# Performance work log

Hardware: AMD Instinct MI355X
Metric: run time of the kernel (lower is better)

The kernel has to match this reference:

```python
import jax, jax.numpy as jnp
import numpy as np

DIM = 256      # d_model (MCMoE default dim=256)
E = 4          # experts: [CoAFusion, SNNFusion, DAMISLFusion, DropX2Fusion]
K = 2          # max_experts (top-k in cosine gate)
ATT = 128      # gated-attention hidden dim in DAMISL MIL pooling
N1, N2, B = 16384, 4096, 1


def setup_inputs() -> dict:
    key = jax.random.key(0)
    ks = jax.random.split(key, 16)
    s = 1.0 / np.sqrt(DIM)
    f32 = jnp.float32
    lin = lambda k, shape, scale: jax.random.normal(k, shape, f32) * scale
    return {
        'x1': jax.random.normal(ks[0], (B, N1, DIM), f32),
        'x2': jax.random.normal(ks[1], (B, N2, DIM), f32),
        # MM_CosineGate params: per-expert prototype rows + activation thresholds
        'sim_matrix': lin(ks[2], (E, DIM), 1.0),
        'gates': jnp.zeros((E,), f32),
        # SNNFusion: RMSNorm scales + two SNN blocks (Linear+ELU)
        'g1': jnp.ones((DIM,), f32),
        'g2': jnp.ones((DIM,), f32),
        'snn_w1': lin(ks[3], (DIM, DIM), s), 'snn_b1': jnp.zeros((DIM,), f32),
        'snn_w2': lin(ks[4], (DIM, DIM), s), 'snn_b2': jnp.zeros((DIM,), f32),
        # CoAFusion: single-head cross attention x1 -> x2
        'wq': lin(ks[5], (DIM, DIM), s), 'wk': lin(ks[6], (DIM, DIM), s),
        'wv': lin(ks[7], (DIM, DIM), s), 'wo': lin(ks[8], (DIM, DIM), s),
        # DAMISLFusion: gated-attention MIL pooling over x2 + fuse linear
        'va': lin(ks[9], (DIM, ATT), s), 'ua': lin(ks[10], (DIM, ATT), s),
        'wa': lin(ks[11], (ATT, 1), 1.0 / np.sqrt(ATT)),
        'wf': lin(ks[12], (DIM, DIM), s),
    }


def _rms(x, g):
    return x * jax.lax.rsqrt(jnp.mean(x * x, axis=-1, keepdims=True) + 1e-6) * g


def _forward(x1, x2, sim_matrix, gates, g1, g2, snn_w1, snn_b1, snn_w2, snn_b2,
             wq, wk, wv, wo, va, ua, wa, wf):
    # ---- MM_CosineGate: cosine similarity of pooled multimodal feature vs prototypes
    f = 0.5 * (x1.mean(axis=1) + x2.mean(axis=1))                       # [B, D]
    fn = f * jax.lax.rsqrt(jnp.sum(f * f, -1, keepdims=True) + 1e-8)
    sn = sim_matrix * jax.lax.rsqrt(jnp.sum(sim_matrix * sim_matrix, -1, keepdims=True) + 1e-8)
    scores = fn @ sn.T                                                  # [B, E]
    topv = jax.lax.top_k(scores, K)[0]                                  # [B, K]
    keep = (scores >= topv[:, -1:]) & (scores > gates[None, :])         # top-k AND above gate
    logits = jnp.where(keep, scores, 0.0)                               # [B, E], 0 for inactive

    # ---- Expert 0: CoAFusion (cross attention, residual)
    attn = jax.nn.softmax(
        jnp.einsum('bnd,bmd->bnm', x1 @ wq, x2 @ wk) / np.sqrt(DIM), axis=-1)  # [B, N1, N2]
    e0 = x1 + jnp.einsum('bnm,bmd->bnd', attn, x2 @ wv) @ wo

    # ---- Expert 1: SNNFusion (per-token SNN on x1 + pooled SNN on x2)
    e1 = jax.nn.elu(_rms(x1, g1) @ snn_w1 + snn_b1) \
         + jax.nn.elu(_rms(x2, g2) @ snn_w2 + snn_b2).mean(axis=1, keepdims=True)

    # ---- Expert 2: DAMISLFusion (gated-attention MIL pool of x2, broadcast fuse)
    h = jnp.tanh(x2 @ va) * jax.nn.sigmoid(x2 @ ua)                     # [B, N2, ATT]
    a = jax.nn.softmax((h @ wa)[..., 0], axis=1)                        # [B, N2]
    pooled = jnp.einsum('bm,bmd->bd', a, x2)                            # [B, D]
    e2 = x1 + (pooled @ wf)[:, None, :]

    # ---- Expert 3: DropX2Fusion (identity on x1)
    e3 = x1

    # ---- Weighted combine over selected experts (weight 0 => expert contributes 0),
    # then divide by number of selected experts (matches `outputs /= num_selected`).
    w = logits
    out = (w[:, 0, None, None] * e0 + w[:, 1, None, None] * e1
           + w[:, 2, None, None] * e2 + w[:, 3, None, None] * e3)
    num_sel = jnp.maximum(jnp.sum(logits > 0, axis=-1), 1).astype(out.dtype)  # [B]
    return out / num_sel[:, None, None]


def reference(x1, x2, sim_matrix, gates, g1, g2, snn_w1, snn_b1, snn_w2, snn_b2,
              wq, wk, wv, wo, va, ua, wa, wf):
    return _forward(x1, x2, sim_matrix, gates, g1, g2, snn_w1, snn_b1,
                    snn_w2, snn_b2, wq, wk, wv, wo, va, ua, wa, wf)
```

## Files before the change

### kernel.cpp

```cpp
#include <hip/hip_runtime.h>
#include <math.h>

#define N1 16384
#define N2 4096
#define DIM 256
#define ATT 128

typedef unsigned int uint32;
typedef __attribute__((ext_vector_type(4))) short s4v;
typedef __attribute__((ext_vector_type(8))) short s8v;
typedef __attribute__((ext_vector_type(16))) float f16v;
typedef __attribute__((ext_vector_type(2))) uint32 u2v;
typedef __attribute__((ext_vector_type(4))) uint32 u4v;

union S8U { s8v v; s4v h[2]; };

#define AS1C const __attribute__((address_space(1)))
#define AS3 __attribute__((address_space(3)))

#define WS_KPK 0
#define WS_VPK 524288
#define WS_WQT 1048576
#define WS_WOT 1081344
#define WS_W1T 1114112
#define WS_WKT 1146880
#define WS_WVT 1179648
#define WS_W2T 1212416
#define WS_VAT 1245184
#define WS_UAT 1261568
#define WS_ACC 1277952
#define WS_COLSUM1 (WS_ACC)
#define WS_COLSUM2 (WS_ACC+256)
#define WS_S2SUM  (WS_ACC+512)
#define WS_POOLED (WS_ACC+768)
#define WS_SUME   (WS_ACC+1024)
#define WS_GATE   (WS_ACC+1040)

#define L_K    0
#define L_V    65536
#define L_P    131072
#define L_LP   147456
#define L_LINV 149504
#define L_RRS  149760
#define L_RR   150016
#define L_CVL  150272
#define L_X1PK  0
#define L_QPAD  65536
#define L_OBUF  0
#define L_X1PK2 65536
#define SMEM_BYTES 151296

__device__ __forceinline__ uint32 f2bf1(float f) {
    uint32 u = __float_as_uint(f);
    return (u + 0x7fffu + ((u >> 16) & 1u)) >> 16;
}
__device__ __forceinline__ uint32 f2bf2(float lo, float hi) {
    return f2bf1(lo) | (f2bf1(hi) << 16);
}
#define MFMA32(a, b, c) __builtin_amdgcn_mfma_f32_32x32x16_bf16((a), (b), (c), 0, 0, 0)

__global__ __launch_bounds__(256) void k_pre(const float* __restrict__ x1,
    const float* __restrict__ x2,
    const float* __restrict__ wq, const float* __restrict__ wo,
    const float* __restrict__ snn_w1, const float* __restrict__ wk,
    const float* __restrict__ wv, const float* __restrict__ snn_w2,
    const float* __restrict__ va, const float* __restrict__ ua,
    const float* __restrict__ g1, const float* __restrict__ g2,
    float* __restrict__ ws)
{
    const int b = blockIdx.x;
    const int t = threadIdx.x;
    if (b < 224) {
        int mat, chunk, ncols;
        if (b < 192) { mat = b >> 5; chunk = b & 31; ncols = 256; }
        else { mat = 6 + ((b - 192) >> 4); chunk = (b - 192) & 15; ncols = 128; }
        const float* W;
        int dstoff;
        switch (mat) {
            case 0: W = wq;     dstoff = WS_WQT; break;
            case 1: W = wo;     dstoff = WS_WOT; break;
            case 2: W = snn_w1; dstoff = WS_W1T; break;
            case 3: W = wk;     dstoff = WS_WKT; break;
            case 4: W = wv;     dstoff = WS_WVT; break;
            case 5: W = snn_w2; dstoff = WS_W2T; break;
            case 6: W = va;     dstoff = WS_VAT; break;
            default: W = ua;    dstoff = WS_UAT; break;
        }
        unsigned short* dst = (unsigned short*)(ws + dstoff);
        const int e0 = chunk * 2048 + t * 8;
        const int k = (ncols == 256) ? (e0 >> 8) : (e0 >> 7);
        const int n0 = (ncols == 256) ? (e0 & 255) : (e0 & 127);
        const float4 v0 = *(const float4*)(W + k * ncols + n0);
        const float4 v1 = *(const float4*)(W + k * ncols + n0 + 4);
        const float sc = (mat == 2) ? g1[k] : ((mat == 5) ? g2[k] : 1.0f);
        float vals[8] = {v0.x, v0.y, v0.z, v0.w, v1.x, v1.y, v1.z, v1.w};
        const unsigned int sbase = (unsigned int)(k >> 4) * 512u
            + 32u * ((k >> 3) & 1) * 8u + (k & 7);
        #pragma unroll
        for (int jj = 0; jj < 8; ++jj) {
            const int n = n0 + jj;
            unsigned int off = (unsigned int)(n >> 5) * 16u * 512u + sbase
                             + (unsigned int)(n & 31) * 8u;
            dst[off] = (unsigned short)f2bf1(vals[jj] * sc);
        }
    } else if (b < 480) {
        const int rbase = (b - 224) * 64;
        float acc = 0.f;
        for (int r = 0; r < 64; ++r) acc += x1[(size_t)(rbase + r) * DIM + t];
        atomicAdd(&ws[WS_COLSUM1 + t], acc);
    } else {
        const int rbase = (b - 480) * 64;
        float acc = 0.f;
        for (int r = 0; r < 64; ++r) acc += x2[(size_t)(rbase + r) * DIM + t];
        atomicAdd(&ws[WS_COLSUM2 + t], acc);
    }
}

__global__ __launch_bounds__(512) void k_mid(const float* __restrict__ x2,
    const float* __restrict__ b2, const float* __restrict__ wa,
    const float* __restrict__ sim, const float* __restrict__ gates,
    float* __restrict__ ws)
{
    __shared__ char xps[16384];
    __shared__ float rrs[32];
    __shared__ float dlp[128];
    __shared__ float expE[32];
    __shared__ float acc9[9];
    const int t = threadIdx.x;
    const int w = t >> 6;
    const int lane = t & 63;
    const int l31 = lane & 31;
    const int lh = lane >> 5;
    const int b = blockIdx.x;

    if (b == 128) {
        if (t < 9) acc9[t] = 0.f;
        __syncthreads();
        float fv = 0.f;
        if (t < 256)
            fv = 0.5f * (ws[WS_COLSUM1 + t] * (1.0f / N1)
                       + ws[WS_COLSUM2 + t] * (1.0f / N2));
        {
            float p = fv * fv;
            #pragma unroll
            for (int o = 32; o > 0; o >>= 1) p += __shfl_xor(p, o);
            if (lane == 0) atomicAdd(&acc9[0], p);
        }
        #pragma unroll
        for (int e = 0; e < 4; ++e) {
            const float sv = (t < 256) ? sim[e * DIM + t] : 0.f;
            float pn = sv * sv, pd = sv * fv;
            #pragma unroll
            for (int o = 32; o > 0; o >>= 1) { pn += __shfl_xor(pn, o); pd += __shfl_xor(pd, o); }
            if (lane == 0) { atomicAdd(&acc9[1 + e], pn); atomicAdd(&acc9[5 + e], pd); }
        }
        __syncthreads();
        if (t == 0) {
            const float rsqf = rsqrtf(acc9[0] + 1e-8f);
            float sc[4];
            #pragma unroll
            for (int e = 0; e < 4; ++e)
                sc[e] = acc9[5 + e] * rsqf * rsqrtf(acc9[1 + e] + 1e-8f);
            float a = -1e30f, bb = -1e30f;
            #pragma unroll
            for (int e = 0; e < 4; ++e) {
                const float v = sc[e];
                if (v > a) { bb = a; a = v; } else if (v > bb) { bb = v; }
            }
            float wv_[4]; int ns = 0;
            #pragma unroll
            for (int e = 0; e < 4; ++e) {
                const bool keep = (sc[e] >= bb) && (sc[e] > gates[e]);
                wv_[e] = keep ? sc[e] : 0.f;
                if (wv_[e] > 0.f) ns++;
            }
            if (ns < 1) ns = 1;
            ws[WS_GATE + 0] = wv_[0]; ws[WS_GATE + 1] = wv_[1];
            ws[WS_GATE + 2] = wv_[2]; ws[WS_GATE + 3] = wv_[3];
            ws[WS_GATE + 4] = 1.0f / (float)ns;
            ws[WS_GATE + 5] = wv_[0] + wv_[2] + wv_[3];
        }
        return;
    }

    const int tb = b * 32;
    unsigned short* kpk = (unsigned short*)(ws + WS_KPK);
    unsigned short* vpk = (unsigned short*)(ws + WS_VPK);
    const char* wsb = (const char*)ws;
    const char* wkt = wsb + (size_t)WS_WKT * 4;
    const char* wvt = wsb + (size_t)WS_WVT * 4;
    const char* w2t = wsb + (size_t)WS_W2T * 4;
    const char* vat = wsb + (size_t)WS_VAT * 4;
    const char* uat = wsb + (size_t)WS_UAT * 4;

    #pragma unroll
    for (int i = 0; i < 2; ++i) {
        const int c = t + 512 * i;
        const int tk = c >> 5, d0 = (c & 31) * 8;
        const float4 a = *(const float4*)(x2 + (size_t)(tb + tk) * DIM + d0);
        const float4 bb = *(const float4*)(x2 + (size_t)(tb + tk) * DIM + d0 + 4);
        float ss = a.x*a.x + a.y*a.y + a.z*a.z + a.w*a.w
                 + bb.x*bb.x + bb.y*bb.y + bb.z*bb.z + bb.w*bb.w;
        #pragma unroll
        for (int o = 16; o > 0; o >>= 1) ss += __shfl_down(ss, o, 32);
        if ((t & 31) == 0) rrs[tk] = ss;
        u4v pk;
        pk.x = f2bf2(a.x, a.y); pk.y = f2bf2(a.z, a.w);
        pk.z = f2bf2(bb.x, bb.y); pk.w = f2bf2(bb.z, bb.w);
        *(u4v*)(xps + (d0 >> 4) * 1024 + (tk + 32 * ((d0 >> 3) & 1)) * 16) = pk;
    }
    __syncthreads();

    {
        f16v kacc = (f16v)0.0f;
        #pragma unroll
        for (int s = 0; s < 16; ++s) {
            const s8v a = *(const s8v*)(wkt + (w * 16 + s) * 1024 + lane * 16);
            const s8v bb = *(const s8v*)(xps + s * 1024 + lane * 16);
            kacc = MFMA32(a, bb, kacc);
        }
        #pragma unroll
        for (int g = 0; g < 4; ++g) {
            const unsigned int chunkK =
                (unsigned int)((b >> 1) * 32 + 2 * (2 * w + (g >> 1)) + (b & 1));
            const unsigned int off = chunkK * 512u
                + (unsigned int)(l31 + 32 * (g & 1)) * 8u + 4u * lh;
            u2v pk;
            pk.x = f2bf2(kacc[4 * g + 0], kacc[4 * g + 1]);
            pk.y = f2bf2(kacc[4 * g + 2], kacc[4 * g + 3]);
            *(u2v*)(kpk + off) = pk;
        }
    }
    {
        f16v vacc = (f16v)0.0f;
        #pragma unroll
        for (int s = 0; s < 16; ++s) {
            const s8v a = *(const s8v*)(xps + s * 1024 + lane * 16);
            const s8v bb = *(const s8v*)(wvt + (w * 16 + s) * 1024 + lane * 16);
            vacc = MFMA32(a, bb, vacc);
        }
        #pragma unroll
        for (int g = 0; g < 4; ++g) {
            const unsigned int chunkV =
                (unsigned int)((b >> 1) * 32 + 4 * w + 2 * (b & 1) + (g >> 1));
            const unsigned int off = chunkV * 512u
                + (unsigned int)(l31 + 32 * (g & 1)) * 8u + 4u * lh;
            u2v pk;
            pk.x = f2bf2(vacc[4 * g + 0], vacc[4 * g + 1]);
            pk.y = f2bf2(vacc[4 * g + 2], vacc[4 * g + 3]);
            *(u2v*)(vpk + off) = pk;
        }
    }
    {
        f16v sacc = (f16v)0.0f;
        #pragma unroll
        for (int s = 0; s < 16; ++s) {
            const s8v a = *(const s8v*)(w2t + (w * 16 + s) * 1024 + lane * 16);
            const s8v bb = *(const s8v*)(xps + s * 1024 + lane * 16);
            sacc = MFMA32(a, bb, sacc);
        }
        const float rrl = rsqrtf(rrs[l31] * (1.0f / DIM) + 1e-6f);
        #pragma unroll
        for (int g = 0; g < 4; ++g) {
            const float4 bb = *(const float4*)(b2 + 32 * w + 8 * g + 4 * lh);
            #pragma unroll
            for (int jj = 0; jj < 4; ++jj) {
                float v = sacc[4 * g + jj] * rrl + ((const float*)&bb)[jj];
                v = (v > 0.f) ? v : expm1f(v);
                v += __shfl_xor(v, 16); v += __shfl_xor(v, 8);
                v += __shfl_xor(v, 4);  v += __shfl_xor(v, 2);
                v += __shfl_xor(v, 1);
                if (l31 == 0)
                    atomicAdd(&ws[WS_S2SUM + 32 * w + 8 * g + 4 * lh + jj], v);
            }
        }
    }
    if (w < 4) {
        f16v hv = (f16v)0.0f, hu = (f16v)0.0f;
        #pragma unroll
        for (int s = 0; s < 16; ++s) {
            const s8v bb = *(const s8v*)(xps + s * 1024 + lane * 16);
            const s8v a1 = *(const s8v*)(vat + (w * 16 + s) * 1024 + lane * 16);
            const s8v a2 = *(const s8v*)(uat + (w * 16 + s) * 1024 + lane * 16);
            hv = MFMA32(a1, bb, hv);
            hu = MFMA32(a2, bb, hu);
        }
        float acc = 0.f;
        #pragma unroll
        for (int g = 0; g < 4; ++g) {
            const float4 w4 = *(const float4*)(wa + 32 * w + 8 * g + 4 * lh);
            #pragma unroll
            for (int jj = 0; jj < 4; ++jj) {
                acc += tanhf(hv[4 * g + jj])
                     * (1.0f / (1.0f + expf(-hu[4 * g + jj])))
                     * ((const float*)&w4)[jj];
            }
        }
        acc += __shfl_xor(acc, 32);
        if (lh == 0) dlp[w * 32 + l31] = acc;
    }
    __syncthreads();
    if (t < 32) {
        const float lg = dlp[t] + dlp[32 + t] + dlp[64 + t] + dlp[96 + t];
        const float e_ = __expf(lg);
        expE[t] = e_;
        float s = e_;
        #pragma unroll
        for (int o = 16; o > 0; o >>= 1) s += __shfl_xor(s, o);
        if (t == 0) atomicAdd(&ws[WS_SUME], s);
    }
    __syncthreads();
    {
        const int d = t & 255, half = t >> 8;
        const int r0 = half * 16;
        float acc = 0.f;
        #pragma unroll
        for (int r = 0; r < 16; ++r)
            acc = fmaf(expE[r0 + r], x2[(size_t)(tb + r0 + r) * DIM + d], acc);
        atomicAdd(&ws[WS_POOLED + d], acc);
    }
}

__global__ __launch_bounds__(512, 2) void k_flash(
    const float* __restrict__ x1, const float* __restrict__ b1,
    const float* __restrict__ wf,
    const float* __restrict__ wsf, float* __restrict__ out)
{
    extern __shared__ char sm[];
    const int t = threadIdx.x;
    const int w = t >> 6;
    const int lane = t & 63;
    const int l31 = lane & 31;
    const int lh = lane >> 5;
    const int qb = blockIdx.x * 64;
    const int kh = w >> 1, qh = w & 1;
    const int qp = w & 1, dpair = w >> 1;
    const char* wsb = (const char*)wsf;
    const char* kpk = wsb + (size_t)WS_KPK * 4;
    const char* vpk = wsb + (size_t)WS_VPK * 4;
    const char* wqt = wsb + (size_t)WS_WQT * 4;
    const char* wot = wsb + (size_t)WS_WOT * 4;
    const char* w1t = wsb + (size_t)WS_W1T * 4;

    auto stage64 = [&](const char* gbase, int ldsoff) {
        #pragma unroll
        for (int i = 0; i < 8; ++i) {
            const int c = w * 8 + i;
            __builtin_amdgcn_global_load_lds(
                (AS1C uint32*)(gbase + c * 1024 + lane * 16),
                (AS3 uint32*)(sm + ldsoff + c * 1024), 16, 0, 0);
        }
    };

    if (t < 256) {
        const float se = wsf[WS_SUME];
        ((float*)(sm + L_LP))[t] = wsf[WS_POOLED + t] / se;
    }
    __syncthreads();
    if (t < 256) {
        const float* pl = (const float*)(sm + L_LP);
        float acc = 0.f;
        for (int k = 0; k < 256; ++k) acc = fmaf(pl[k], wf[k * DIM + t], acc);
        ((float*)(sm + L_CVL))[t] = wsf[WS_GATE + 1] * (wsf[WS_S2SUM + t] * (1.0f / N2))
                                  + wsf[WS_GATE + 2] * acc;
    }

    #pragma unroll
    for (int i = 0; i < 4; ++i) {
        const int c = t + 512 * i;
        const int q = c >> 5, d0 = (c & 31) * 8;
        const float4 a = *(const float4*)(x1 + (size_t)(qb + q) * DIM + d0);
        const float4 bb = *(const float4*)(x1 + (size_t)(qb + q) * DIM + d0 + 4);
        float ss = a.x*a.x + a.y*a.y + a.z*a.z + a.w*a.w
                 + bb.x*bb.x + bb.y*bb.y + bb.z*bb.z + bb.w*bb.w;
        #pragma unroll
        for (int o = 16; o > 0; o >>= 1) ss += __shfl_down(ss, o, 32);
        if ((t & 31) == 0) *(float*)(sm + L_RRS + q * 4) = ss;
        u4v pk;
        pk.x = f2bf2(a.x, a.y); pk.y = f2bf2(a.z, a.w);
        pk.z = f2bf2(bb.x, bb.y); pk.w = f2bf2(bb.z, bb.w);
        *(u4v*)(sm + L_X1PK + ((q >> 5) * 16 + (d0 >> 4)) * 1024
                + ((q & 31) + 32 * ((d0 >> 3) & 1)) * 16) = pk;
    }
    __syncthreads();
    if (t < 64) {
        const float s2 = *(const float*)(sm + L_RRS + t * 4);
        *(float*)(sm + L_RR + t * 4) = rsqrtf(s2 * (1.0f / DIM) + 1e-6f);
    }
    #pragma unroll
    for (int i = 0; i < 2; ++i) {
        const int mt = w, qt = i;
        f16v qa = (f16v)0.0f;
        #pragma unroll
        for (int s = 0; s < 16; ++s) {
            const s8v a  = *(const s8v*)(wqt + (mt * 16 + s) * 1024 + lane * 16);
            const s8v bb = *(const s8v*)(sm + L_X1PK + (qt * 16 + s) * 1024 + lane * 16);
            qa = MFMA32(a, bb, qa);
        }
        const int q = qt * 32 + l31;
        #pragma unroll
        for (int g = 0; g < 4; ++g) {
            const int d0 = 32 * mt + 8 * g + 4 * lh;
            u2v pk;
            pk.x = f2bf2(qa[4 * g + 0], qa[4 * g + 1]);
            pk.y = f2bf2(qa[4 * g + 2], qa[4 * g + 3]);
            *(u2v*)(sm + L_QPAD + q * 520 + d0 * 2) = pk;
        }
    }
    __syncthreads();
    s8v qf[16];
    {
        const char* qbase = sm + L_QPAD + (qh * 32 + l31) * 520 + lh * 16;
        #pragma unroll
        for (int s = 0; s < 16; ++s) {
            S8U u;
            u.h[0] = *(const s4v*)(qbase + s * 32);
            u.h[1] = *(const s4v*)(qbase + s * 32 + 8);
            qf[s] = u.v;
        }
    }
    stage64(kpk, L_K);
    __syncthreads();

    f16v oacc0 = (f16v)0.0f, oacc1 = (f16v)0.0f;
    float lsum = 0.0f;

    for (int tile = 0; tile < 32; ++tile) {
        stage64(vpk + (size_t)tile * 65536, L_V);
        f16v sacc = (f16v)0.0f;
        #pragma unroll
        for (int s = 0; s < 16; ++s) {
            const s8v a = *(const s8v*)(sm + L_K
                + ((kh >> 1) * 32 + 2 * s + (kh & 1)) * 1024 + lane * 16);
            sacc = MFMA32(a, qf[s], sacc);
        }
        #pragma unroll
        for (int g = 0; g < 4; ++g) {
            const float p0 = __expf(sacc[4 * g + 0] * 0.0625f);
            const float p1 = __expf(sacc[4 * g + 1] * 0.0625f);
            const float p2 = __expf(sacc[4 * g + 2] * 0.0625f);
            const float p3 = __expf(sacc[4 * g + 3] * 0.0625f);
            lsum += (p0 + p1) + (p2 + p3);
            const int keyo = 32 * kh + 8 * g + 4 * lh;
            const int kc = keyo >> 4, ko = keyo & 15;
            u2v pk; pk.x = f2bf2(p0, p1); pk.y = f2bf2(p2, p3);
            *(u2v*)(sm + L_P + (qh * 8 + kc) * 1024
                    + (l31 + 32 * (ko >> 3)) * 16 + (ko & 7) * 2) = pk;
        }
        __syncthreads();
        if (tile < 31) stage64(kpk + (size_t)(tile + 1) * 65536, L_K);
        s8v pf[8];
        #pragma unroll
        for (int kc = 0; kc < 8; ++kc)
            pf[kc] = *(const s8v*)(sm + L_P + (qp * 8 + kc) * 1024 + lane * 16);
        #pragma unroll
        for (int kc = 0; kc < 8; ++kc) {
            const int sub = (kc >> 2) * 32, k3 = kc & 3;
            const s8v a0 = *(const s8v*)(sm + L_V + (sub + 4 * (2 * dpair) + k3) * 1024 + lane * 16);
            const s8v a1 = *(const s8v*)(sm + L_V + (sub + 4 * (2 * dpair + 1) + k3) * 1024 + lane * 16);
            oacc0 = MFMA32(a0, pf[kc], oacc0);
            oacc1 = MFMA32(a1, pf[kc], oacc1);
        }
        __syncthreads();
    }

    *(float*)(sm + L_LP + ((w * 2 + lh) * 32 + l31) * 4) = lsum;
    __syncthreads();
    if (t < 64) {
        const int qh_ = t >> 5, c = t & 31;
        const float* lp = (const float*)(sm + L_LP);
        float l = 0.f;
        #pragma unroll
        for (int k2 = 0; k2 < 4; ++k2)
            l += lp[((k2 * 2 + qh_) * 2 + 0) * 32 + c]
               + lp[((k2 * 2 + qh_) * 2 + 1) * 32 + c];
        *(float*)(sm + L_LINV + t * 4) = 1.0f / l;
    }
    __syncthreads();
    {
        const float li = *(const float*)(sm + L_LINV + (qp * 32 + l31) * 4);
        #pragma unroll
        for (int half = 0; half < 2; ++half) {
            const f16v acc = half ? oacc1 : oacc0;
            const int dc = 2 * dpair + half;
            #pragma unroll
            for (int g = 0; g < 4; ++g) {
                const int d0 = dc * 32 + 8 * g + 4 * lh;
                u2v pk;
                pk.x = f2bf2(acc[4 * g + 0] * li, acc[4 * g + 1] * li);
                pk.y = f2bf2(acc[4 * g + 2] * li, acc[4 * g + 3] * li);
                *(u2v*)(sm + L_OBUF + (qp * 16 + (d0 >> 4)) * 1024
                        + (l31 + 32 * ((d0 >> 3) & 1)) * 16 + (d0 & 7) * 2) = pk;
            }
        }
    }
    #pragma unroll
    for (int i = 0; i < 4; ++i) {
        const int c = t + 512 * i;
        const int q = c >> 5, d0 = (c & 31) * 8;
        const float4 a = *(const float4*)(x1 + (size_t)(qb + q) * DIM + d0);
        const float4 bb = *(const float4*)(x1 + (size_t)(qb + q) * DIM + d0 + 4);
        u4v pk;
        pk.x = f2bf2(a.x, a.y); pk.y = f2bf2(a.z, a.w);
        pk.z = f2bf2(bb.x, bb.y); pk.w = f2bf2(bb.z, bb.w);
        *(u4v*)(sm + L_X1PK2 + ((q >> 5) * 16 + (d0 >> 4)) * 1024
                + ((q & 31) + 32 * ((d0 >> 3) & 1)) * 16) = pk;
    }
    __syncthreads();
    const float gw0 = wsf[WS_GATE + 0], gw1 = wsf[WS_GATE + 1];
    const float ginv = wsf[WS_GATE + 4], gcx1 = wsf[WS_GATE + 5];
    #pragma unroll
    for (int i = 0; i < 2; ++i) {
        const int mt = w, qt = i;
        f16v ea = (f16v)0.0f, sa = (f16v)0.0f;
        for (int s = 0; s < 16; ++s) {
            const s8v awo = *(const s8v*)(wot + (mt * 16 + s) * 1024 + lane * 16);
            const s8v aw1 = *(const s8v*)(w1t + (mt * 16 + s) * 1024 + lane * 16);
            const s8v bo = *(const s8v*)(sm + L_OBUF + (qt * 16 + s) * 1024 + lane * 16);
            const s8v bx = *(const s8v*)(sm + L_X1PK2 + (qt * 16 + s) * 1024 + lane * 16);
            ea = MFMA32(awo, bo, ea);
            sa = MFMA32(aw1, bx, sa);
        }
        const int q = qt * 32 + l31;
        const float rrq = *(const float*)(sm + L_RR + q * 4);
        #pragma unroll
        for (int g = 0; g < 4; ++g) {
            const int d0 = 32 * mt + 8 * g + 4 * lh;
            const float4 cv = *(const float4*)(sm + L_CVL + d0 * 4);
            const float4 bb = *(const float4*)(b1 + d0);
            const float4 xx = *(const float4*)(x1 + (size_t)(qb + q) * DIM + d0);
            float ev0 = sa[4 * g + 0] * rrq + bb.x; ev0 = (ev0 > 0.f) ? ev0 : expm1f(ev0);
            float ev1 = sa[4 * g + 1] * rrq + bb.y; ev1 = (ev1 > 0.f) ? ev1 : expm1f(ev1);
            float ev2 = sa[4 * g + 2] * rrq + bb.z; ev2 = (ev2 > 0.f) ? ev2 : expm1f(ev2);
            float ev3 = sa[4 * g + 3] * rrq + bb.w; ev3 = (ev3 > 0.f) ? ev3 : expm1f(ev3);
            float4 o;
            o.x = ginv * (gcx1 * xx.x + gw0 * ea[4 * g + 0] + gw1 * ev0 + cv.x);
            o.y = ginv * (gcx1 * xx.y + gw0 * ea[4 * g + 1] + gw1 * ev1 + cv.y);
            o.z = ginv * (gcx1 * xx.z + gw0 * ea[4 * g + 2] + gw1 * ev2 + cv.z);
            o.w = ginv * (gcx1 * xx.w + gw0 * ea[4 * g + 3] + gw1 * ev3 + cv.w);
            *(float4*)(out + (size_t)(qb + q) * DIM + d0) = o;
        }
    }
}

extern "C" void kernel_launch(void* const* d_in, const int* in_sizes, int n_in,
                              void* d_out, int out_size, void* d_ws, size_t ws_size,
                              hipStream_t stream)
{
    (void)in_sizes; (void)n_in; (void)out_size; (void)ws_size;
    const float* x1    = (const float*)d_in[0];
    const float* x2    = (const float*)d_in[1];
    const float* sim   = (const float*)d_in[2];
    const float* gates = (const float*)d_in[3];
    const float* g1    = (const float*)d_in[4];
    const float* g2    = (const float*)d_in[5];
    const float* w1m   = (const float*)d_in[6];
    const float* b1    = (const float*)d_in[7];
    const float* w2m   = (const float*)d_in[8];
    const float* b2    = (const float*)d_in[9];
    const float* wq    = (const float*)d_in[10];
    const float* wk    = (const float*)d_in[11];
    const float* wv    = (const float*)d_in[12];
    const float* wo    = (const float*)d_in[13];
    const float* va    = (const float*)d_in[14];
    const float* ua    = (const float*)d_in[15];
    const float* wa    = (const float*)d_in[16];
    const float* wf    = (const float*)d_in[17];
    float* ws  = (float*)d_ws;
    float* out = (float*)d_out;

    hipMemsetAsync(ws + WS_ACC, 0, 1056 * sizeof(float), stream);
    hipLaunchKernelGGL(k_pre, dim3(544), dim3(256), 0, stream,
                       x1, x2, wq, wo, w1m, wk, wv, w2m, va, ua, g1, g2, ws);
    hipLaunchKernelGGL(k_mid, dim3(129), dim3(512), 0, stream,
                       x2, b2, wa, sim, gates, ws);
    hipLaunchKernelGGL(k_flash, dim3(N1 / 64), dim3(512), SMEM_BYTES, stream,
                       x1, b1, wf, ws, out);
}
```

Measured before the change: 251.1 us.

## Switch flash attention K, V, Q, P operands to FP8 MFMA and precompute pooled projection

Stores the K and V projections, the Q fragments and the softmax probabilities as FP8 instead of BF16. Attention now uses the fp8 32x32x16 MFMA, which halves global staging bytes, LDS tile sizes and total shared memory, so two blocks can fit per CU. The pooled@wf matvec moves from every k_flash block into k_mid, using linearity to accumulate per-block projected partials atomically. It also uses __expf in the gated attention. The cost is lower numerical precision in the attention path, and the older fp8 MFMA may have lower throughput than the bf16 one.

```diff
diff --git a/kernel.cpp b/kernel.cpp
--- a/kernel.cpp
+++ b/kernel.cpp
@@ -19,36 +19,36 @@
 #define AS3 __attribute__((address_space(3)))
 
 #define WS_KPK 0
-#define WS_VPK 524288
-#define WS_WQT 1048576
-#define WS_WOT 1081344
-#define WS_W1T 1114112
-#define WS_WKT 1146880
-#define WS_WVT 1179648
-#define WS_W2T 1212416
-#define WS_VAT 1245184
-#define WS_UAT 1261568
-#define WS_ACC 1277952
+#define WS_VPK 262144
+#define WS_WQT 524288
+#define WS_WOT 557056
+#define WS_W1T 589824
+#define WS_WKT 622592
+#define WS_WVT 655360
+#define WS_W2T 688128
+#define WS_VAT 720896
+#define WS_UAT 737280
+#define WS_ACC 753664
 #define WS_COLSUM1 (WS_ACC)
 #define WS_COLSUM2 (WS_ACC+256)
 #define WS_S2SUM  (WS_ACC+512)
-#define WS_POOLED (WS_ACC+768)
+#define WS_CVRAW  (WS_ACC+768)
 #define WS_SUME   (WS_ACC+1024)
 #define WS_GATE   (WS_ACC+1040)
 
 #define L_K    0
-#define L_V    65536
-#define L_P    131072
-#define L_LP   147456
-#define L_LINV 149504
-#define L_RRS  149760
-#define L_RR   150016
-#define L_CVL  150272
+#define L_V    32768
+#define L_P    65536
+#define L_LP   73728
+#define L_LINV 75776
+#define L_RRS  76032
+#define L_RR   76288
+#define L_CVL  76544
 #define L_X1PK  0
-#define L_QPAD  65536
+#define L_QPAD  32768
 #define L_OBUF  0
-#define L_X1PK2 65536
-#define SMEM_BYTES 151296
+#define L_X1PK2 32768
+#define SMEM_BYTES 77568
 
 __device__ __forceinline__ uint32 f2bf1(float f) {
     uint32 u = __float_as_uint(f);
@@ -57,7 +57,13 @@
 __device__ __forceinline__ uint32 f2bf2(float lo, float hi) {
     return f2bf1(lo) | (f2bf1(hi) << 16);
 }
+__device__ __forceinline__ uint32 f2fp8x4(float a, float b, float c, float d) {
+    uint32 r = __builtin_amdgcn_cvt_pk_fp8_f32(a, b, 0, 0);
+    r = __builtin_amdgcn_cvt_pk_fp8_f32(c, d, r, 1);
+    return r;
+}
 #define MFMA32(a, b, c) __builtin_amdgcn_mfma_f32_32x32x16_bf16((a), (b), (c), 0, 0, 0)
+#define MFMA8(a, b, c)  __builtin_amdgcn_mfma_f32_32x32x16_fp8_fp8((a), (b), (c), 0, 0, 0)
 
 __global__ __launch_bounds__(256) void k_pre(const float* __restrict__ x1,
     const float* __restrict__ x2,
@@ -119,6 +125,7 @@
 __global__ __launch_bounds__(512) void k_mid(const float* __restrict__ x2,
     const float* __restrict__ b2, const float* __restrict__ wa,
     const float* __restrict__ sim, const float* __restrict__ gates,
+    const float* __restrict__ wf,
     float* __restrict__ ws)
 {
     __shared__ char xps[16384];
@@ -126,6 +133,8 @@
     __shared__ float dlp[128];
     __shared__ float expE[32];
     __shared__ float acc9[9];
+    __shared__ float pph[512];
+    __shared__ float pbv[256];
     const int t = threadIdx.x;
     const int w = t >> 6;
     const int lane = t & 63;
@@ -184,8 +193,8 @@
     }
 
     const int tb = b * 32;
-    unsigned short* kpk = (unsigned short*)(ws + WS_KPK);
-    unsigned short* vpk = (unsigned short*)(ws + WS_VPK);
+    unsigned char* kpk = (unsigned char*)(ws + WS_KPK);
+    unsigned char* vpk = (unsigned char*)(ws + WS_VPK);
     const char* wsb = (const char*)ws;
     const char* wkt = wsb + (size_t)WS_WKT * 4;
     const char* wvt = wsb + (size_t)WS_WVT * 4;
@@ -225,10 +234,7 @@
                 (unsigned int)((b >> 1) * 32 + 2 * (2 * w + (g >> 1)) + (b & 1));
             const unsigned int off = chunkK * 512u
                 + (unsigned int)(l31 + 32 * (g & 1)) * 8u + 4u * lh;
-            u2v pk;
-            pk.x = f2bf2(kacc[4 * g + 0], kacc[4 * g + 1]);
-            pk.y = f2bf2(kacc[4 * g + 2], kacc[4 * g + 3]);
-            *(u2v*)(kpk + off) = pk;
+            *(uint32*)(kpk + off) = f2fp8x4(kacc[4*g+0], kacc[4*g+1], kacc[4*g+2], kacc[4*g+3]);
         }
     }
     {
@@ -245,10 +251,7 @@
                 (unsigned int)((b >> 1) * 32 + 4 * w + 2 * (b & 1) + (g >> 1));
             const unsigned int off = chunkV * 512u
                 + (unsigned int)(l31 + 32 * (g & 1)) * 8u + 4u * lh;
-            u2v pk;
-            pk.x = f2bf2(vacc[4 * g + 0], vacc[4 * g + 1]);
-            pk.y = f2bf2(vacc[4 * g + 2], vacc[4 * g + 3]);
-            *(u2v*)(vpk + off) = pk;
+            *(uint32*)(vpk + off) = f2fp8x4(vacc[4*g+0], vacc[4*g+1], vacc[4*g+2], vacc[4*g+3]);
         }
     }
     {
@@ -292,7 +295,7 @@
             #pragma unroll
             for (int jj = 0; jj < 4; ++jj) {
                 acc += tanhf(hv[4 * g + jj])
-                     * (1.0f / (1.0f + expf(-hu[4 * g + jj])))
+                     * (1.0f / (1.0f + __expf(-hu[4 * g + jj])))
                      * ((const float*)&w4)[jj];
             }
         }
@@ -317,13 +320,25 @@
         #pragma unroll
         for (int r = 0; r < 16; ++r)
             acc = fmaf(expE[r0 + r], x2[(size_t)(tb + r0 + r) * DIM + d], acc);
-        atomicAdd(&ws[WS_POOLED + d], acc);
-    }
+        pph[t] = acc;
+    }
+    __syncthreads();
+    if (t < 256) pbv[t] = pph[t] + pph[t + 256];
+    __syncthreads();
+    {
+        const int o = t & 255, h2 = t >> 8;
+        float ca = 0.f;
+        #pragma unroll 4
+        for (int d2 = h2 * 128; d2 < h2 * 128 + 128; ++d2)
+            ca = fmaf(pbv[d2], wf[d2 * DIM + o], ca);
+        pph[t] = ca;
+    }
+    __syncthreads();
+    if (t < 256) atomicAdd(&ws[WS_CVRAW + t], pph[t] + pph[t + 256]);
 }
 
 __global__ __launch_bounds__(512, 2) void k_flash(
     const float* __restrict__ x1, const float* __restrict__ b1,
-    const float* __restrict__ wf,
     const float* __restrict__ wsf, float* __restrict__ out)
 {
     extern __shared__ char sm[];
@@ -342,10 +357,10 @@
     const char* wot = wsb + (size_t)WS_WOT * 4;
     const char* w1t = wsb + (size_t)WS_W1T * 4;
 
-    auto stage64 = [&](const char* gbase, int ldsoff) {
-        #pragma unroll
-        for (int i = 0; i < 8; ++i) {
-            const int c = w * 8 + i;
+    auto stage32 = [&](const char* gbase, int ldsoff) {
+        #pragma unroll
+        for (int i = 0; i < 4; ++i) {
+            const int c = w * 4 + i;
             __builtin_amdgcn_global_load_lds(
                 (AS1C uint32*)(gbase + c * 1024 + lane * 16),
                 (AS3 uint32*)(sm + ldsoff + c * 1024), 16, 0, 0);
@@ -354,15 +369,9 @@
 
     if (t < 256) {
         const float se = wsf[WS_SUME];
-        ((float*)(sm + L_LP))[t] = wsf[WS_POOLED + t] / se;
-    }
-    __syncthreads();
-    if (t < 256) {
-        const float* pl = (const float*)(sm + L_LP);
-        float acc = 0.f;
-        for (int k = 0; k < 256; ++k) acc = fmaf(pl[k], wf[k * DIM + t], acc);
-        ((float*)(sm + L_CVL))[t] = wsf[WS_GATE + 1] * (wsf[WS_S2SUM + t] * (1.0f / N2))
-                                  + wsf[WS_GATE + 2] * acc;
+        ((float*)(sm + L_CVL))[t] =
+            wsf[WS_GATE + 1] * (wsf[WS_S2SUM + t] * (1.0f / N2))
+          + wsf[WS_GATE + 2] * (wsf[WS_CVRAW + t] / se);
     }
 
     #pragma unroll
@@ -401,38 +410,32 @@
         #pragma unroll
         for (int g = 0; g < 4; ++g) {
             const int d0 = 32 * mt + 8 * g + 4 * lh;
-            u2v pk;
-            pk.x = f2bf2(qa[4 * g + 0], qa[4 * g + 1]);
-            pk.y = f2bf2(qa[4 * g + 2], qa[4 * g + 3]);
-            *(u2v*)(sm + L_QPAD + q * 520 + d0 * 2) = pk;
-        }
-    }
-    __syncthreads();
-    s8v qf[16];
-    {
-        const char* qbase = sm + L_QPAD + (qh * 32 + l31) * 520 + lh * 16;
-        #pragma unroll
-        for (int s = 0; s < 16; ++s) {
-            S8U u;
-            u.h[0] = *(const s4v*)(qbase + s * 32);
-            u.h[1] = *(const s4v*)(qbase + s * 32 + 8);
-            qf[s] = u.v;
-        }
-    }
-    stage64(kpk, L_K);
+            *(uint32*)(sm + L_QPAD + q * 264 + d0) =
+                f2fp8x4(qa[4*g+0], qa[4*g+1], qa[4*g+2], qa[4*g+3]);
+        }
+    }
+    __syncthreads();
+    long qf[16];
+    {
+        const char* qbase = sm + L_QPAD + (qh * 32 + l31) * 264 + lh * 8;
+        #pragma unroll
+        for (int s = 0; s < 16; ++s)
+            qf[s] = *(const long*)(qbase + s * 16);
+    }
+    stage32(kpk, L_K);
     __syncthreads();
 
     f16v oacc0 = (f16v)0.0f, oacc1 = (f16v)0.0f;
     float lsum = 0.0f;
 
     for (int tile = 0; tile < 32; ++tile) {
-        stage64(vpk + (size_t)tile * 65536, L_V);
+        stage32(vpk + (size_t)tile * 32768, L_V);
         f16v sacc = (f16v)0.0f;
         #pragma unroll
         for (int s = 0; s < 16; ++s) {
-            const s8v a = *(const s8v*)(sm + L_K
-                + ((kh >> 1) * 32 + 2 * s + (kh & 1)) * 1024 + lane * 16);
-            sacc = MFMA32(a, qf[s], sacc);
+            const long a = *(const long*)(sm + L_K
+                + ((kh >> 1) * 32 + 2 * s + (kh & 1)) * 512 + lane * 8);
+            sacc = MFMA8(a, qf[s], sacc);
         }
         #pragma unroll
         for (int g = 0; g < 4; ++g) {
@@ -443,23 +446,23 @@
             lsum += (p0 + p1) + (p2 + p3);
             const int keyo = 32 * kh + 8 * g + 4 * lh;
             const int kc = keyo >> 4, ko = keyo & 15;
-            u2v pk; pk.x = f2bf2(p0, p1); pk.y = f2bf2(p2, p3);
-            *(u2v*)(sm + L_P + (qh * 8 + kc) * 1024
-                    + (l31 + 32 * (ko >> 3)) * 16 + (ko & 7) * 2) = pk;
+            *(uint32*)(sm + L_P + (qh * 8 + kc) * 512
+                       + (l31 + 32 * (ko >> 3)) * 8 + (ko & 7)) =
+                f2fp8x4(p0, p1, p2, p3);
         }
         __syncthreads();
-        if (tile < 31) stage64(kpk + (size_t)(tile + 1) * 65536, L_K);
-        s8v pf[8];
+        if (tile < 31) stage32(kpk + (size_t)(tile + 1) * 32768, L_K);
+        long pf[8];
         #pragma unroll
         for (int kc = 0; kc < 8; ++kc)
-            pf[kc] = *(const s8v*)(sm + L_P + (qp * 8 + kc) * 1024 + lane * 16);
+            pf[kc] = *(const long*)(sm + L_P + (qp * 8 + kc) * 512 + lane * 8);
         #pragma unroll
         for (int kc = 0; kc < 8; ++kc) {
             const int sub = (kc >> 2) * 32, k3 = kc & 3;
-            const s8v a0 = *(const s8v*)(sm + L_V + (sub + 4 * (2 * dpair) + k3) * 1024 + lane * 16);
-            const s8v a1 = *(const s8v*)(sm + L_V + (sub + 4 * (2 * dpair + 1) + k3) * 1024 + lane * 16);
-            oacc0 = MFMA32(a0, pf[kc], oacc0);
-            oacc1 = MFMA32(a1, pf[kc], oacc1);
+            const long a0 = *(const long*)(sm + L_V + (sub + 4 * (2 * dpair) + k3) * 512 + lane * 8);
+            const long a1 = *(const long*)(sm + L_V + (sub + 4 * (2 * dpair + 1) + k3) * 512 + lane * 8);
+            oacc0 = MFMA8(a0, pf[kc], oacc0);
+            oacc1 = MFMA8(a1, pf[kc], oacc1);
         }
         __syncthreads();
     }
@@ -573,7 +576,7 @@
     hipLaunchKernelGGL(k_pre, dim3(544), dim3(256), 0, stream,
                        x1, x2, wq, wo, w1m, wk, wv, w2m, va, ua, g1, g2, ws);
     hipLaunchKernelGGL(k_mid, dim3(129), dim3(512), 0, stream,
-                       x2, b2, wa, sim, gates, ws);
+                       x2, b2, wa, sim, gates, wf, ws);
     hipLaunchKernelGGL(k_flash, dim3(N1 / 64), dim3(512), SMEM_BYTES, stream,
-                       x1, b1, wf, ws, out);
-}
+                       x1, b1, ws, out);
+}
```

Measured after the change: 228.9 us. -8.8%, faster.
